# Kernel optimization log

Hardware: AMD Instinct MI355X
Metric: run time of the kernel (lower is better)

## Reference

```python
import jax, jax.numpy as jnp
import numpy as np

D_MODEL = 2048
NUM_HEADS = 32
NUM_KV_HEADS = 8
HEAD_DIM = D_MODEL // NUM_HEADS  # 64
KV_DIM = NUM_KV_HEADS * HEAD_DIM  # 512


def setup_inputs() -> dict:
    key = jax.random.key(0)
    ks = jax.random.split(key, 9)
    s = 1.0 / np.sqrt(D_MODEL)
    x = jax.random.normal(ks[0], (4, 1024, D_MODEL), dtype=jnp.float32)
    Wq = jax.random.uniform(ks[1], (D_MODEL, D_MODEL), jnp.float32, -s, s)
    bq = jax.random.uniform(ks[2], (D_MODEL,), jnp.float32, -s, s)
    Wk = jax.random.uniform(ks[3], (D_MODEL, KV_DIM), jnp.float32, -s, s)
    bk = jax.random.uniform(ks[4], (KV_DIM,), jnp.float32, -s, s)
    Wv = jax.random.uniform(ks[5], (D_MODEL, KV_DIM), jnp.float32, -s, s)
    bv = jax.random.uniform(ks[6], (KV_DIM,), jnp.float32, -s, s)
    Wo = jax.random.uniform(ks[7], (D_MODEL, D_MODEL), jnp.float32, -s, s)
    bo = jax.random.uniform(ks[8], (D_MODEL,), jnp.float32, -s, s)
    return {"x": x, "Wq": Wq, "bq": bq, "Wk": Wk, "bk": bk,
            "Wv": Wv, "bv": bv, "Wo": Wo, "bo": bo}


def reference(x, Wq, bq, Wk, bk, Wv, bv, Wo, bo):
    B, S, _ = x.shape
    g = NUM_HEADS // NUM_KV_HEADS  # heads per kv head
    # projections
    q = (x @ Wq + bq).reshape(B, S, NUM_HEADS, HEAD_DIM).transpose(0, 2, 1, 3)   # [B,H,S,d]
    k = (x @ Wk + bk).reshape(B, S, NUM_KV_HEADS, HEAD_DIM).transpose(0, 2, 1, 3)  # [B,Hkv,S,d]
    v = (x @ Wv + bv).reshape(B, S, NUM_KV_HEADS, HEAD_DIM).transpose(0, 2, 1, 3)
    # repeat_interleave KV heads across query-head groups
    k = jnp.repeat(k, g, axis=1)  # [B,H,S,d]
    v = jnp.repeat(v, g, axis=1)
    scores = jnp.einsum('bhqd,bhkd->bhqk', q, k) / np.sqrt(HEAD_DIM)  # [B,H,S,S]
    attn = jax.nn.softmax(scores, axis=-1)
    ctx = jnp.einsum('bhqk,bhkd->bhqd', attn, v)  # [B,H,S,d]
    ctx = ctx.transpose(0, 2, 1, 3).reshape(B, S, D_MODEL)
    return ctx @ Wo + bo
```

## Files before the change

kernel.cpp:

```cpp
#include <hip/hip_runtime.h>
#include <stdint.h>

typedef unsigned short u16;
typedef __attribute__((ext_vector_type(8))) __bf16 bf16x8;
typedef __attribute__((ext_vector_type(4))) __bf16 bf16x4;
typedef __attribute__((ext_vector_type(4))) float f32x4;

#define QSCALE 0.1803368801111204f

#if __has_builtin(__builtin_amdgcn_exp2f)
#define EXP2(x) __builtin_amdgcn_exp2f(x)
#else
#define EXP2(x) exp2f(x)
#endif

__device__ __forceinline__ u16 f2bf(float f) {
  uint32_t u = __float_as_uint(f);
  u += 0x7fffu + ((u >> 16) & 1u);
  return (u16)(u >> 16);
}
__device__ __forceinline__ float bf2f(u16 h) {
  return __uint_as_float(((uint32_t)h) << 16);
}
__device__ __forceinline__ uint32_t pack2bf(float a, float b) {
  return (uint32_t)f2bf(a) | ((uint32_t)f2bf(b) << 16);
}

__device__ __forceinline__ void gl_lds16(const u16* g, u16* l) {
  __builtin_amdgcn_global_load_lds(
      (const __attribute__((address_space(1))) unsigned int*)g,
      (__attribute__((address_space(3))) unsigned int*)l, 16, 0, 0);
}

__global__ void detect_dtype(const u16* __restrict__ x, int* __restrict__ flag) {
  __shared__ int any_huge;
  if (threadIdx.x == 0) any_huge = 0;
  __syncthreads();
  int huge = 0;
  for (int i = threadIdx.x; i < 4096; i += 256) {
    float v = bf2f(x[i]);
    if (!(fabsf(v) < 1e6f)) huge = 1;
  }
  if (huge) any_huge = 1;
  __syncthreads();
  if (threadIdx.x == 0) *flag = any_huge;
}

__global__ __launch_bounds__(256) void prep(
    const void* __restrict__ Wq, const void* __restrict__ Wk,
    const void* __restrict__ Wv, const void* __restrict__ Wo,
    const void* __restrict__ x,
    const void* __restrict__ bq, const void* __restrict__ bk,
    const void* __restrict__ bv, const void* __restrict__ bo,
    u16* __restrict__ WT, u16* __restrict__ WoT, u16* __restrict__ xb,
    float* __restrict__ biasf, const int* __restrict__ flag) {
  const int fl = *flag;
  int id = blockIdx.x;
  const int tid = threadIdx.x;
  if (id < 2560) {
    __shared__ u16 tile[64 * 72];
    const void* in; u16* outp; int N, rowoff;
    if (id < 1024)      { in = Wq; outp = WT;  N = 2048; rowoff = 0; }
    else if (id < 1280) { in = Wk; outp = WT;  N = 512;  rowoff = 2048; id -= 1024; }
    else if (id < 1536) { in = Wv; outp = WT;  N = 512;  rowoff = 2560; id -= 1280; }
    else                { in = Wo; outp = WoT; N = 2048; rowoff = 0;    id -= 1536; }
    int tiles_x = N >> 6;
    int nb = (id % tiles_x) * 64, kb = (id / tiles_x) * 64;
    const int kbase = (tid >> 4) * 4, nc = (tid & 15) * 4;
    if (fl) {
      float4 L[4];
#pragma unroll
      for (int p = 0; p < 4; ++p)
        L[p] = *(const float4*)&((const float*)in)[(size_t)(kb + kbase + p) * N + nb + nc];
#pragma unroll
      for (int nj = 0; nj < 4; ++nj) {
        uint2 w;
        w.x = pack2bf(((const float*)&L[0])[nj], ((const float*)&L[1])[nj]);
        w.y = pack2bf(((const float*)&L[2])[nj], ((const float*)&L[3])[nj]);
        *(uint2*)&tile[(nc + nj) * 72 + kbase] = w;
      }
    } else {
      uint2 L[4];
#pragma unroll
      for (int p = 0; p < 4; ++p)
        L[p] = *(const uint2*)&((const u16*)in)[(size_t)(kb + kbase + p) * N + nb + nc];
#pragma unroll
      for (int nj = 0; nj < 4; ++nj) {
        uint2 w;
        w.x = (uint32_t)((const u16*)&L[0])[nj] | ((uint32_t)((const u16*)&L[1])[nj] << 16);
        w.y = (uint32_t)((const u16*)&L[2])[nj] | ((uint32_t)((const u16*)&L[3])[nj] << 16);
        *(uint2*)&tile[(nc + nj) * 72 + kbase] = w;
      }
    }
    __syncthreads();
#pragma unroll
    for (int it = 0; it < 2; ++it) {
      int sid = it * 256 + tid;
      int row = sid >> 3, kseg = (sid & 7) * 8;
      uint4 v = *(const uint4*)&tile[row * 72 + kseg];
      *(uint4*)&outp[(size_t)(rowoff + nb + row) * 2048 + kb + kseg] = v;
    }
  } else if (id < 4608) {
    size_t base = ((size_t)(id - 2560) * 256 + tid) * 16;
    if (fl) {
      const float* xf = (const float*)x;
      float4 a = *(const float4*)&xf[base];
      float4 b = *(const float4*)&xf[base + 4];
      float4 c = *(const float4*)&xf[base + 8];
      float4 d = *(const float4*)&xf[base + 12];
      uint4 o0, o1;
      o0.x = pack2bf(a.x, a.y); o0.y = pack2bf(a.z, a.w);
      o0.z = pack2bf(b.x, b.y); o0.w = pack2bf(b.z, b.w);
      o1.x = pack2bf(c.x, c.y); o1.y = pack2bf(c.z, c.w);
      o1.z = pack2bf(d.x, d.y); o1.w = pack2bf(d.z, d.w);
      *(uint4*)&xb[base] = o0;
      *(uint4*)&xb[base + 8] = o1;
    } else {
      const u16* x16 = (const u16*)x;
      *(uint4*)&xb[base] = *(const uint4*)&x16[base];
      *(uint4*)&xb[base + 8] = *(const uint4*)&x16[base + 8];
    }
  } else {
    int i = (id - 4608) * 256 + tid;
    if (i < 5120) {
      const void* src; int idx;
      if (i < 2048)      { src = bq; idx = i; }
      else if (i < 2560) { src = bk; idx = i - 2048; }
      else if (i < 3072) { src = bv; idx = i - 2560; }
      else               { src = bo; idx = i - 3072; }
      biasf[i] = fl ? ((const float*)src)[idx] : bf2f(((const u16*)src)[idx]);
    }
  }
}

template <bool SWAP>
__device__ __forceinline__ void gemm_loop(
    const u16* __restrict__ A, const u16* __restrict__ BT,
    u16* __restrict__ Al, u16* __restrict__ Bl,
    int m0, int n0, int K, int tid, f32x4 acc[4][4]) {
  const int wave = tid >> 6, lane = tid & 63;
  const int ln = lane & 15, quad = lane >> 4;
  const int wm = (wave >> 1) * 64, wn = (wave & 1) * 64;
  const int sw8 = (quad ^ ((ln >> 1) & 3)) * 8;

  const int c0 = wave * 128 + lane, c1 = c0 + 64;
  const int kq0 = ((c0 & 3) ^ ((c0 >> 3) & 3)) * 8;
  const int kq1 = ((c1 & 3) ^ ((c1 >> 3) & 3)) * 8;
  const u16* a0 = &A[(size_t)(m0 + (c0 >> 2)) * K + kq0];
  const u16* a1 = &A[(size_t)(m0 + (c1 >> 2)) * K + kq1];
  const u16* b0 = &BT[(size_t)(n0 + (c0 >> 2)) * K + kq0];
  const u16* b1 = &BT[(size_t)(n0 + (c1 >> 2)) * K + kq1];

  for (int kt = 0; kt < K; kt += 32) {
    __syncthreads();
    gl_lds16(a0 + kt, &Al[c0 * 8]);
    gl_lds16(a1 + kt, &Al[c1 * 8]);
    gl_lds16(b0 + kt, &Bl[c0 * 8]);
    gl_lds16(b1 + kt, &Bl[c1 * 8]);
    __asm__ volatile("s_waitcnt vmcnt(0)" ::: "memory");
    __syncthreads();
    bf16x8 af[4], bfr[4];
#pragma unroll
    for (int i = 0; i < 4; ++i)
      af[i] = *(const bf16x8*)&Al[(wm + i * 16 + ln) * 32 + sw8];
#pragma unroll
    for (int j = 0; j < 4; ++j)
      bfr[j] = *(const bf16x8*)&Bl[(wn + j * 16 + ln) * 32 + sw8];
#pragma unroll
    for (int i = 0; i < 4; ++i)
#pragma unroll
      for (int j = 0; j < 4; ++j)
        acc[i][j] = SWAP
            ? __builtin_amdgcn_mfma_f32_16x16x32_bf16(bfr[j], af[i], acc[i][j], 0, 0, 0)
            : __builtin_amdgcn_mfma_f32_16x16x32_bf16(af[i], bfr[j], acc[i][j], 0, 0, 0);
  }
}

__global__ __launch_bounds__(256) void gemm_qkv(
    const u16* __restrict__ A, const u16* __restrict__ BT,
    const float* __restrict__ bias,
    u16* __restrict__ qo, u16* __restrict__ ko, u16* __restrict__ vo, int K) {
  __shared__ u16 Al[128 * 32];
  __shared__ u16 Bl[128 * 32];
  const int tid = threadIdx.x;
  const int wave = tid >> 6, lane = tid & 63;
  const int ln = lane & 15, quad = lane >> 4;
  const int m0 = blockIdx.y * 128, n0 = blockIdx.x * 128;
  const int wm = (wave >> 1) * 64, wn = (wave & 1) * 64;

  f32x4 acc[4][4];
#pragma unroll
  for (int i = 0; i < 4; ++i)
#pragma unroll
    for (int j = 0; j < 4; ++j) acc[i][j] = {0.f, 0.f, 0.f, 0.f};

  if (blockIdx.x < 20) {
    gemm_loop<true>(A, BT, Al, Bl, m0, n0, K, tid, acc);
    const bool isq = (n0 < 2048);
#pragma unroll
    for (int j = 0; j < 4; ++j) {
      int nbase = n0 + wn + j * 16 + quad * 4;
      float4 bsv = *(const float4*)&bias[nbase];
      int n2 = isq ? nbase : nbase - 2048;
      int h = n2 >> 6, dd = n2 & 63;
      u16* o = isq ? qo : ko;
      int hmul = isq ? 32 : 8;
#pragma unroll
      for (int i = 0; i < 4; ++i) {
        int m = m0 + wm + i * 16 + ln;
        int b = m >> 10, s = m & 1023;
        float v0 = acc[i][j][0] + bsv.x, v1 = acc[i][j][1] + bsv.y;
        float v2 = acc[i][j][2] + bsv.z, v3 = acc[i][j][3] + bsv.w;
        if (isq) { v0 *= QSCALE; v1 *= QSCALE; v2 *= QSCALE; v3 *= QSCALE; }
        uint2 st; st.x = pack2bf(v0, v1); st.y = pack2bf(v2, v3);
        *(uint2*)&o[(((size_t)(b * hmul + h)) * 1024 + s) * 64 + dd] = st;
      }
    }
  } else {
    gemm_loop<false>(A, BT, Al, Bl, m0, n0, K, tid, acc);
#pragma unroll
    for (int j = 0; j < 4; ++j) {
      int gn = n0 + wn + j * 16 + ln;
      float bs = bias[gn];
      int n2 = gn - 2560, h = n2 >> 6, dd = n2 & 63;
#pragma unroll
      for (int i = 0; i < 4; ++i) {
        int mb = m0 + wm + i * 16 + quad * 4;
        int b = mb >> 10, sb = mb & 1023;
        uint2 st;
        st.x = pack2bf(acc[i][j][0] + bs, acc[i][j][1] + bs);
        st.y = pack2bf(acc[i][j][2] + bs, acc[i][j][3] + bs);
        *(uint2*)&vo[(((size_t)(b * 8 + h)) * 64 + dd) * 1024 + sb] = st;
      }
    }
  }
}

__global__ __launch_bounds__(256) void gemm_o(
    const u16* __restrict__ A, const u16* __restrict__ BT,
    const float* __restrict__ bias, u16* __restrict__ o0,
    int N, int K, const int* __restrict__ flag) {
  __shared__ u16 Al[128 * 32];
  __shared__ u16 Bl[128 * 32];
  const int tid = threadIdx.x;
  const int wave = tid >> 6, lane = tid & 63;
  const int ln = lane & 15, quad = lane >> 4;
  const int m0 = blockIdx.y * 128, n0 = blockIdx.x * 128;
  const int wm = (wave >> 1) * 64, wn = (wave & 1) * 64;
  const int fl = *flag;

  f32x4 acc[4][4];
#pragma unroll
  for (int i = 0; i < 4; ++i)
#pragma unroll
    for (int j = 0; j < 4; ++j) acc[i][j] = {0.f, 0.f, 0.f, 0.f};

  gemm_loop<true>(A, BT, Al, Bl, m0, n0, K, tid, acc);

#pragma unroll
  for (int j = 0; j < 4; ++j) {
    int nbase = n0 + wn + j * 16 + quad * 4;
    float4 bsv = *(const float4*)&bias[nbase];
#pragma unroll
    for (int i = 0; i < 4; ++i) {
      int m = m0 + wm + i * 16 + ln;
      float v0 = acc[i][j][0] + bsv.x, v1 = acc[i][j][1] + bsv.y;
      float v2 = acc[i][j][2] + bsv.z, v3 = acc[i][j][3] + bsv.w;
      if (fl) {
        float4 st = {v0, v1, v2, v3};
        *(float4*)&((float*)o0)[(size_t)m * N + nbase] = st;
      } else {
        uint2 st; st.x = pack2bf(v0, v1); st.y = pack2bf(v2, v3);
        *(uint2*)&o0[(size_t)m * N + nbase] = st;
      }
    }
  }
}

__global__ __launch_bounds__(256) void attn_kernel(
    const u16* __restrict__ q_ws, const u16* __restrict__ k_ws,
    const u16* __restrict__ vt_ws, u16* __restrict__ ctx) {
  __shared__ u16 Kl[64 * 72];
  __shared__ u16 Vl[64 * 72];
  __shared__ u16 Pl[4 * 16 * 68];
  const int tid = threadIdx.x;
  const int wave = tid >> 6, lane = tid & 63;
  const int ln = lane & 15, quad = lane >> 4;
  const int qt = blockIdx.x;
  const int bh = blockIdx.y;
  const int b = bh >> 5, h = bh & 31, kvh = h >> 2;
  const int q0 = qt * 64;
  const size_t qbase = (size_t)bh * 1024 * 64;
  const u16* kptr = k_ws + (size_t)(b * 8 + kvh) * 1024 * 64;
  const u16* vptr = vt_ws + (size_t)(b * 8 + kvh) * 64 * 1024;

  const int qrow = q0 + wave * 16 + ln;
  bf16x8 qf0 = *(const bf16x8*)&q_ws[qbase + (size_t)qrow * 64 + quad * 8];
  bf16x8 qf1 = *(const bf16x8*)&q_ws[qbase + (size_t)qrow * 64 + 32 + quad * 8];

  float lsum = 0.f;
  f32x4 oacc[4];
#pragma unroll
  for (int t = 0; t < 4; ++t) oacc[t] = {0.f, 0.f, 0.f, 0.f};

  const int kr0 = tid >> 3, kp0 = (tid & 7) * 8;
  const int kr1 = kr0 + 32;
  const int prow = wave * 16 * 68 + ln * 68;

  uint4 kv0 = *(const uint4*)&kptr[(size_t)kr0 * 64 + kp0];
  uint4 kv1 = *(const uint4*)&kptr[(size_t)kr1 * 64 + kp0];
  uint4 vv0 = *(const uint4*)&vptr[(size_t)kr0 * 1024 + kp0];
  uint4 vv1 = *(const uint4*)&vptr[(size_t)kr1 * 1024 + kp0];

  for (int kb = 0; kb < 1024; kb += 64) {
    __syncthreads();
    *(uint4*)&Kl[kr0 * 72 + kp0] = kv0;
    *(uint4*)&Kl[kr1 * 72 + kp0] = kv1;
    *(uint4*)&Vl[kr0 * 72 + kp0] = vv0;
    *(uint4*)&Vl[kr1 * 72 + kp0] = vv1;
    __syncthreads();

    {
      int nkb = (kb + 64) & 1023;
      kv0 = *(const uint4*)&kptr[(size_t)(nkb + kr0) * 64 + kp0];
      kv1 = *(const uint4*)&kptr[(size_t)(nkb + kr1) * 64 + kp0];
      vv0 = *(const uint4*)&vptr[(size_t)kr0 * 1024 + nkb + kp0];
      vv1 = *(const uint4*)&vptr[(size_t)kr1 * 1024 + nkb + kp0];
    }

    f32x4 sacc[4];
#pragma unroll
    for (int t = 0; t < 4; ++t) sacc[t] = {0.f, 0.f, 0.f, 0.f};
#pragma unroll
    for (int t = 0; t < 4; ++t) {
      bf16x8 kf0 = *(const bf16x8*)&Kl[(t * 16 + ln) * 72 + quad * 8];
      bf16x8 kf1 = *(const bf16x8*)&Kl[(t * 16 + ln) * 72 + 32 + quad * 8];
      sacc[t] = __builtin_amdgcn_mfma_f32_16x16x32_bf16(kf0, qf0, sacc[t], 0, 0, 0);
      sacc[t] = __builtin_amdgcn_mfma_f32_16x16x32_bf16(kf1, qf1, sacc[t], 0, 0, 0);
    }

    uint2 pk[4];
#pragma unroll
    for (int t = 0; t < 4; ++t) {
      float p0 = EXP2(sacc[t][0]);
      float p1 = EXP2(sacc[t][1]);
      float p2 = EXP2(sacc[t][2]);
      float p3 = EXP2(sacc[t][3]);
      lsum += (p0 + p1) + (p2 + p3);
      pk[t].x = __builtin_amdgcn_perm(__float_as_uint(p1), __float_as_uint(p0), 0x07060302u);
      pk[t].y = __builtin_amdgcn_perm(__float_as_uint(p3), __float_as_uint(p2), 0x07060302u);
    }
#pragma unroll
    for (int t = 0; t < 4; ++t)
      *(uint2*)&Pl[prow + t * 16 + quad * 4] = pk[t];
    __asm__ volatile("s_waitcnt lgkmcnt(0)" ::: "memory");

    bf16x8 pf0 = *(const bf16x8*)&Pl[prow + quad * 8];
    bf16x8 pf1 = *(const bf16x8*)&Pl[prow + 32 + quad * 8];

#pragma unroll
    for (int t = 0; t < 4; ++t) {
      bf16x8 vf0 = *(const bf16x8*)&Vl[(t * 16 + ln) * 72 + quad * 8];
      bf16x8 vf1 = *(const bf16x8*)&Vl[(t * 16 + ln) * 72 + 32 + quad * 8];
      oacc[t] = __builtin_amdgcn_mfma_f32_16x16x32_bf16(vf0, pf0, oacc[t], 0, 0, 0);
      oacc[t] = __builtin_amdgcn_mfma_f32_16x16x32_bf16(vf1, pf1, oacc[t], 0, 0, 0);
    }
  }

  float l2 = lsum + __shfl_xor(lsum, 16);
  l2 += __shfl_xor(l2, 32);
  const float inv = 1.0f / l2;

  const size_t obase = (size_t)(b * 1024 + qrow) * 2048 + h * 64;
#pragma unroll
  for (int t = 0; t < 4; ++t) {
    uint2 st;
    st.x = pack2bf(oacc[t][0] * inv, oacc[t][1] * inv);
    st.y = pack2bf(oacc[t][2] * inv, oacc[t][3] * inv);
    *(uint2*)&ctx[obase + t * 16 + quad * 4] = st;
  }
}

extern "C" void kernel_launch(void* const* d_in, const int* in_sizes, int n_in,
                              void* d_out, int out_size, void* d_ws, size_t ws_size,
                              hipStream_t stream) {
  const void* x  = d_in[0];
  const void* Wq = d_in[1];
  const void* bq = d_in[2];
  const void* Wk = d_in[3];
  const void* bk = d_in[4];
  const void* Wv = d_in[5];
  const void* bv = d_in[6];
  const void* Wo = d_in[7];
  const void* bo = d_in[8];
  char* ws = (char*)d_ws;

  u16* WT    = (u16*)(ws + 0);
  u16* WoT   = (u16*)(ws + 12582912);
  u16* q_ws  = (u16*)(ws + 20971520);
  u16* k_ws  = (u16*)(ws + 37748736);
  u16* vt_ws = (u16*)(ws + 41943040);
  u16* c_ws  = (u16*)(ws + 46137344);
  u16* xb    = (u16*)(ws + 62914560);
  float* biasf = (float*)(ws + 79691776);
  int* flag  = (int*)(ws + 79712256);

  detect_dtype<<<1, 256, 0, stream>>>((const u16*)x, flag);
  prep<<<4628, 256, 0, stream>>>(Wq, Wk, Wv, Wo, x, bq, bk, bv, bo,
                                 WT, WoT, xb, biasf, flag);

  gemm_qkv<<<dim3(24, 32), 256, 0, stream>>>(xb, WT, biasf, q_ws, k_ws, vt_ws, 2048);
  attn_kernel<<<dim3(16, 128), 256, 0, stream>>>(q_ws, k_ws, vt_ws, c_ws);
  gemm_o<<<dim3(16, 32), 256, 0, stream>>>(c_ws, WoT, biasf + 3072,
                                           (u16*)d_out, 2048, 2048, flag);
}
```

Measured before the change: 303.5 us.

## Rewrite projection GEMMs as 256x256 tiles with double-buffered LDS pipeline

Replaces the 128x128, 4-wave, single-buffered GEMM loop with a 256x256, 8-wave kernel that takes K=64 per stage, double-buffers A and B in 128 KB of LDS, and interleaves global-to-LDS prefetch with MFMA quadrants under explicit barriers and setprio. It targets the exposed load latency and per-K-step syncs of the old loop and raises arithmetic intensity per tile. In exchange, grids shrink to 192 and 128 blocks on a 256-CU part, leaving CUs idle, and K=2048 plus the row stride are now hardcoded.

```diff
diff --git a/kernel.cpp b/kernel.cpp
--- a/kernel.cpp
+++ b/kernel.cpp
@@ -31,6 +31,12 @@
       (const __attribute__((address_space(1))) unsigned int*)g,
       (__attribute__((address_space(3))) unsigned int*)l, 16, 0, 0);
 }
+
+#define S_BAR() __builtin_amdgcn_s_barrier()
+#define LGKM0() do { __asm__ volatile("s_waitcnt lgkmcnt(0)" ::: "memory"); \
+                     __builtin_amdgcn_sched_barrier(0); } while (0)
+#define VMC(N) do { __asm__ volatile("s_waitcnt vmcnt(" #N ")" ::: "memory"); \
+                    __builtin_amdgcn_sched_barrier(0); } while (0)
 
 __global__ void detect_dtype(const u16* __restrict__ x, int* __restrict__ flag) {
   __shared__ int any_huge;
@@ -134,144 +140,196 @@
 }
 
 template <bool SWAP>
-__device__ __forceinline__ void gemm_loop(
-    const u16* __restrict__ A, const u16* __restrict__ BT,
-    u16* __restrict__ Al, u16* __restrict__ Bl,
-    int m0, int n0, int K, int tid, f32x4 acc[4][4]) {
+__device__ __forceinline__ void gemm_loop256(
+    const u16* __restrict__ gA, const u16* __restrict__ gB,
+    u16* __restrict__ lds, int tid, f32x4 (&acc)[8][4]) {
   const int wave = tid >> 6, lane = tid & 63;
   const int ln = lane & 15, quad = lane >> 4;
-  const int wm = (wave >> 1) * 64, wn = (wave & 1) * 64;
-  const int sw8 = (quad ^ ((ln >> 1) & 3)) * 8;
-
-  const int c0 = wave * 128 + lane, c1 = c0 + 64;
-  const int kq0 = ((c0 & 3) ^ ((c0 >> 3) & 3)) * 8;
-  const int kq1 = ((c1 & 3) ^ ((c1 >> 3) & 3)) * 8;
-  const u16* a0 = &A[(size_t)(m0 + (c0 >> 2)) * K + kq0];
-  const u16* a1 = &A[(size_t)(m0 + (c1 >> 2)) * K + kq1];
-  const u16* b0 = &BT[(size_t)(n0 + (c0 >> 2)) * K + kq0];
-  const u16* b1 = &BT[(size_t)(n0 + (c1 >> 2)) * K + kq1];
-
-  for (int kt = 0; kt < K; kt += 32) {
-    __syncthreads();
-    gl_lds16(a0 + kt, &Al[c0 * 8]);
-    gl_lds16(a1 + kt, &Al[c1 * 8]);
-    gl_lds16(b0 + kt, &Bl[c0 * 8]);
-    gl_lds16(b1 + kt, &Bl[c1 * 8]);
-    __asm__ volatile("s_waitcnt vmcnt(0)" ::: "memory");
-    __syncthreads();
-    bf16x8 af[4], bfr[4];
-#pragma unroll
-    for (int i = 0; i < 4; ++i)
-      af[i] = *(const bf16x8*)&Al[(wm + i * 16 + ln) * 32 + sw8];
-#pragma unroll
-    for (int j = 0; j < 4; ++j)
-      bfr[j] = *(const bf16x8*)&Bl[(wn + j * 16 + ln) * 32 + sw8];
-#pragma unroll
-    for (int i = 0; i < 4; ++i)
-#pragma unroll
-      for (int j = 0; j < 4; ++j)
-        acc[i][j] = SWAP
-            ? __builtin_amdgcn_mfma_f32_16x16x32_bf16(bfr[j], af[i], acc[i][j], 0, 0, 0)
-            : __builtin_amdgcn_mfma_f32_16x16x32_bf16(af[i], bfr[j], acc[i][j], 0, 0, 0);
-  }
-}
-
-__global__ __launch_bounds__(256) void gemm_qkv(
+  const int sw8 = 8 * (quad ^ ((ln >> 1) & 3));
+  const int wm = (wave >> 2) * 128, wn = (wave & 3) * 64;
+
+  u16* const A0b = lds;
+  u16* const A1b = lds + 16384;
+  u16* const B0b = lds + 32768;
+  u16* const B1b = lds + 49152;
+
+  const int srow = wave * 16 + (lane >> 2);
+  const int skq = 8 * ((lane & 3) ^ ((lane >> 3) & 3));
+  const u16* const sa = gA + (size_t)srow * 2048 + skq;
+  const u16* const sb = gB + (size_t)srow * 2048 + skq;
+  const int dchunk = (wave * 64 + lane) * 8;
+
+  auto stage = [&](const u16* g, u16* dbase, int H, int kt) {
+    const u16* s = g + (size_t)H * (128 * 2048) + kt;
+    u16* d = dbase + H * 4096 + dchunk;
+    gl_lds16(s, d);
+    gl_lds16(s + 32, d + 8192);
+  };
+
+  bf16x8 af0[8], af1[8], blo[4], bhi[4];
+  auto rdA = [&](bf16x8* dst, const u16* buf, int ibase) {
+#pragma unroll
+    for (int ii = 0; ii < 4; ++ii) {
+      const int ro = (wm + (ibase + ii) * 16 + ln) * 32 + sw8;
+      dst[ii * 2 + 0] = *(const bf16x8*)&buf[ro];
+      dst[ii * 2 + 1] = *(const bf16x8*)&buf[8192 + ro];
+    }
+  };
+  auto rdB = [&](bf16x8* dst, const u16* buf, int jbase) {
+#pragma unroll
+    for (int jj = 0; jj < 2; ++jj) {
+      const int ro = (wn + (jbase + jj) * 16 + ln) * 32 + sw8;
+      dst[jj * 2 + 0] = *(const bf16x8*)&buf[ro];
+      dst[jj * 2 + 1] = *(const bf16x8*)&buf[8192 + ro];
+    }
+  };
+  auto mmaQ = [&](int i0, int j0, const bf16x8* a, const bf16x8* b) {
+#pragma unroll
+    for (int ii = 0; ii < 4; ++ii)
+#pragma unroll
+      for (int jj = 0; jj < 2; ++jj)
+#pragma unroll
+        for (int kh = 0; kh < 2; ++kh) {
+          f32x4& c = acc[i0 + ii][j0 + jj];
+          c = SWAP ? __builtin_amdgcn_mfma_f32_16x16x32_bf16(b[jj * 2 + kh], a[ii * 2 + kh], c, 0, 0, 0)
+                   : __builtin_amdgcn_mfma_f32_16x16x32_bf16(a[ii * 2 + kh], b[jj * 2 + kh], c, 0, 0, 0);
+        }
+  };
+
+  stage(sa, A0b, 0, 0); stage(sa, A0b, 1, 0);
+  stage(sb, B0b, 0, 0); stage(sb, B0b, 1, 0);
+  stage(sa, A1b, 0, 64); stage(sa, A1b, 1, 64);
+  __asm__ volatile("s_waitcnt vmcnt(4)" ::: "memory");
+  S_BAR();
+
+#pragma unroll 1
+  for (int it = 0; it < 16; ++it) {
+    const int kk = it * 128;
+#pragma unroll
+    for (int h = 0; h < 2; ++h) {
+      u16* const Ab = h ? A1b : A0b;
+      u16* const Bb = h ? B1b : B0b;
+      u16* const Bo = h ? B0b : B1b;
+      const int kB = (kk + 64 + h * 64) & 2047;
+      const int kA = (kk + 128 + h * 64) & 2047;
+      rdA(af0, Ab, 0); rdB(blo, Bb, 0);
+      stage(sb, Bo, 0, kB);
+      S_BAR(); LGKM0();
+      __builtin_amdgcn_s_setprio(1); mmaQ(0, 0, af0, blo); __builtin_amdgcn_s_setprio(0);
+      S_BAR();
+      rdA(af1, Ab, 4);
+      stage(sb, Bo, 1, kB);
+      S_BAR(); LGKM0();
+      __builtin_amdgcn_s_setprio(1); mmaQ(4, 0, af1, blo); __builtin_amdgcn_s_setprio(0);
+      S_BAR();
+      rdB(bhi, Bb, 2);
+      stage(sa, Ab, 0, kA);
+      S_BAR(); LGKM0();
+      __builtin_amdgcn_s_setprio(1); mmaQ(4, 2, af1, bhi); __builtin_amdgcn_s_setprio(0);
+      S_BAR();
+      stage(sa, Ab, 1, kA);
+      S_BAR();
+      __builtin_amdgcn_s_setprio(1); mmaQ(0, 2, af0, bhi); __builtin_amdgcn_s_setprio(0);
+      VMC(4);
+      S_BAR();
+    }
+  }
+}
+
+__global__ __launch_bounds__(512, 2) void gemm_qkv(
     const u16* __restrict__ A, const u16* __restrict__ BT,
     const float* __restrict__ bias,
-    u16* __restrict__ qo, u16* __restrict__ ko, u16* __restrict__ vo, int K) {
-  __shared__ u16 Al[128 * 32];
-  __shared__ u16 Bl[128 * 32];
+    u16* __restrict__ qo, u16* __restrict__ ko, u16* __restrict__ vo) {
+  __shared__ __align__(16) u16 lds[65536];
   const int tid = threadIdx.x;
   const int wave = tid >> 6, lane = tid & 63;
   const int ln = lane & 15, quad = lane >> 4;
-  const int m0 = blockIdx.y * 128, n0 = blockIdx.x * 128;
-  const int wm = (wave >> 1) * 64, wn = (wave & 1) * 64;
-
-  f32x4 acc[4][4];
-#pragma unroll
-  for (int i = 0; i < 4; ++i)
+  const int wm = (wave >> 2) * 128, wn = (wave & 3) * 64;
+  const int m0 = blockIdx.y * 256, n0 = blockIdx.x * 256;
+
+  f32x4 acc[8][4];
+#pragma unroll
+  for (int i = 0; i < 8; ++i)
 #pragma unroll
     for (int j = 0; j < 4; ++j) acc[i][j] = {0.f, 0.f, 0.f, 0.f};
 
-  if (blockIdx.x < 20) {
-    gemm_loop<true>(A, BT, Al, Bl, m0, n0, K, tid, acc);
+  if (blockIdx.x < 10) {
+    gemm_loop256<true>(A + (size_t)m0 * 2048, BT + (size_t)n0 * 2048, lds, tid, acc);
     const bool isq = (n0 < 2048);
+    u16* const o = isq ? qo : ko;
+    const int hmul = isq ? 32 : 8;
 #pragma unroll
     for (int j = 0; j < 4; ++j) {
-      int nbase = n0 + wn + j * 16 + quad * 4;
-      float4 bsv = *(const float4*)&bias[nbase];
-      int n2 = isq ? nbase : nbase - 2048;
-      int h = n2 >> 6, dd = n2 & 63;
-      u16* o = isq ? qo : ko;
-      int hmul = isq ? 32 : 8;
-#pragma unroll
-      for (int i = 0; i < 4; ++i) {
-        int m = m0 + wm + i * 16 + ln;
-        int b = m >> 10, s = m & 1023;
+      const int nbase = n0 + wn + j * 16 + quad * 4;
+      const float4 bsv = *(const float4*)&bias[nbase];
+      const int n2 = isq ? nbase : nbase - 2048;
+      const int hh = n2 >> 6, dd = n2 & 63;
+#pragma unroll
+      for (int i = 0; i < 8; ++i) {
+        const int m = m0 + wm + i * 16 + ln;
+        const int b = m >> 10, s = m & 1023;
         float v0 = acc[i][j][0] + bsv.x, v1 = acc[i][j][1] + bsv.y;
         float v2 = acc[i][j][2] + bsv.z, v3 = acc[i][j][3] + bsv.w;
         if (isq) { v0 *= QSCALE; v1 *= QSCALE; v2 *= QSCALE; v3 *= QSCALE; }
         uint2 st; st.x = pack2bf(v0, v1); st.y = pack2bf(v2, v3);
-        *(uint2*)&o[(((size_t)(b * hmul + h)) * 1024 + s) * 64 + dd] = st;
+        *(uint2*)&o[(((size_t)(b * hmul + hh)) * 1024 + s) * 64 + dd] = st;
       }
     }
   } else {
-    gemm_loop<false>(A, BT, Al, Bl, m0, n0, K, tid, acc);
+    gemm_loop256<false>(A + (size_t)m0 * 2048, BT + (size_t)n0 * 2048, lds, tid, acc);
 #pragma unroll
     for (int j = 0; j < 4; ++j) {
-      int gn = n0 + wn + j * 16 + ln;
-      float bs = bias[gn];
-      int n2 = gn - 2560, h = n2 >> 6, dd = n2 & 63;
-#pragma unroll
-      for (int i = 0; i < 4; ++i) {
-        int mb = m0 + wm + i * 16 + quad * 4;
-        int b = mb >> 10, sb = mb & 1023;
+      const int gn = n0 + wn + j * 16 + ln;
+      const float bs = bias[gn];
+      const int n2 = gn - 2560, hh = n2 >> 6, dd = n2 & 63;
+#pragma unroll
+      for (int i = 0; i < 8; ++i) {
+        const int mb = m0 + wm + i * 16 + quad * 4;
+        const int b = mb >> 10, sb = mb & 1023;
         uint2 st;
         st.x = pack2bf(acc[i][j][0] + bs, acc[i][j][1] + bs);
         st.y = pack2bf(acc[i][j][2] + bs, acc[i][j][3] + bs);
-        *(uint2*)&vo[(((size_t)(b * 8 + h)) * 64 + dd) * 1024 + sb] = st;
+        *(uint2*)&vo[(((size_t)(b * 8 + hh)) * 64 + dd) * 1024 + sb] = st;
       }
     }
   }
 }
 
-__global__ __launch_bounds__(256) void gemm_o(
+__global__ __launch_bounds__(512, 2) void gemm_o(
     const u16* __restrict__ A, const u16* __restrict__ BT,
     const float* __restrict__ bias, u16* __restrict__ o0,
-    int N, int K, const int* __restrict__ flag) {
-  __shared__ u16 Al[128 * 32];
-  __shared__ u16 Bl[128 * 32];
+    const int* __restrict__ flag) {
+  __shared__ __align__(16) u16 lds[65536];
   const int tid = threadIdx.x;
   const int wave = tid >> 6, lane = tid & 63;
   const int ln = lane & 15, quad = lane >> 4;
-  const int m0 = blockIdx.y * 128, n0 = blockIdx.x * 128;
-  const int wm = (wave >> 1) * 64, wn = (wave & 1) * 64;
+  const int wm = (wave >> 2) * 128, wn = (wave & 3) * 64;
+  const int m0 = blockIdx.y * 256, n0 = blockIdx.x * 256;
   const int fl = *flag;
 
-  f32x4 acc[4][4];
-#pragma unroll
-  for (int i = 0; i < 4; ++i)
+  f32x4 acc[8][4];
+#pragma unroll
+  for (int i = 0; i < 8; ++i)
 #pragma unroll
     for (int j = 0; j < 4; ++j) acc[i][j] = {0.f, 0.f, 0.f, 0.f};
 
-  gemm_loop<true>(A, BT, Al, Bl, m0, n0, K, tid, acc);
+  gemm_loop256<true>(A + (size_t)m0 * 2048, BT + (size_t)n0 * 2048, lds, tid, acc);
 
 #pragma unroll
   for (int j = 0; j < 4; ++j) {
-    int nbase = n0 + wn + j * 16 + quad * 4;
-    float4 bsv = *(const float4*)&bias[nbase];
-#pragma unroll
-    for (int i = 0; i < 4; ++i) {
-      int m = m0 + wm + i * 16 + ln;
+    const int nbase = n0 + wn + j * 16 + quad * 4;
+    const float4 bsv = *(const float4*)&bias[nbase];
+#pragma unroll
+    for (int i = 0; i < 8; ++i) {
+      const int m = m0 + wm + i * 16 + ln;
       float v0 = acc[i][j][0] + bsv.x, v1 = acc[i][j][1] + bsv.y;
       float v2 = acc[i][j][2] + bsv.z, v3 = acc[i][j][3] + bsv.w;
       if (fl) {
         float4 st = {v0, v1, v2, v3};
-        *(float4*)&((float*)o0)[(size_t)m * N + nbase] = st;
+        *(float4*)&((float*)o0)[(size_t)m * 2048 + nbase] = st;
       } else {
         uint2 st; st.x = pack2bf(v0, v1); st.y = pack2bf(v2, v3);
-        *(uint2*)&o0[(size_t)m * N + nbase] = st;
+        *(uint2*)&o0[(size_t)m * 2048 + nbase] = st;
       }
     }
   }
@@ -409,8 +467,7 @@
   prep<<<4628, 256, 0, stream>>>(Wq, Wk, Wv, Wo, x, bq, bk, bv, bo,
                                  WT, WoT, xb, biasf, flag);
 
-  gemm_qkv<<<dim3(24, 32), 256, 0, stream>>>(xb, WT, biasf, q_ws, k_ws, vt_ws, 2048);
+  gemm_qkv<<<dim3(12, 16), 512, 0, stream>>>(xb, WT, biasf, q_ws, k_ws, vt_ws);
   attn_kernel<<<dim3(16, 128), 256, 0, stream>>>(q_ws, k_ws, vt_ws, c_ws);
-  gemm_o<<<dim3(16, 32), 256, 0, stream>>>(c_ws, WoT, biasf + 3072,
-                                           (u16*)d_out, 2048, 2048, flag);
-}
+  gemm_o<<<dim3(8, 16), 512, 0, stream>>>(c_ws, WoT, biasf + 3072, (u16*)d_out, flag);
+}
```

Result: faster. 294.3 us (-3.0%).
